# Kernel optimization log

Hardware: AMD Instinct MI355X
Metric: run time of the kernel (lower is better)

Reference implementation:

```python
import jax, jax.numpy as jnp
import numpy as np


def setup_inputs() -> dict:
    key = jax.random.key(0)
    kq, kk, kv = jax.random.split(key, 3)
    B, S, D = 8, 2048, 128
    Q = jax.random.normal(kq, (B, S, D), dtype=jnp.float32)
    K = jax.random.normal(kk, (B, S, D), dtype=jnp.float32)
    V = jax.random.normal(kv, (B, S, D), dtype=jnp.float32)
    return {"Q": Q, "K": K, "V": V}


def reference(Q, K, V):
    # scores: [B, S, S]
    d = Q.shape[-1]
    scores = jnp.einsum('bqd,bkd->bqk', Q, K) / jnp.sqrt(jnp.float32(d))
    # causal mask: position i attends to keys <= i (original sets upper triangle to -inf)
    S = scores.shape[-1]
    causal = jnp.tril(jnp.ones((S, S), dtype=bool))  # [S, S]
    scores = jnp.where(causal[None, :, :], scores, -jnp.inf)
    probs = jax.nn.softmax(scores, axis=-1)
    return jnp.einsum('bqk,bkd->bqd', probs, V)
```

## Files before the change

kernel.cpp:

```cpp
#include <hip/hip_runtime.h>

#define BB 8
#define SS 2048
#define DD 128
#define SEG ((size_t)BB * SS * DD)

typedef _Float16 f16;
typedef _Float16 f16x2 __attribute__((ext_vector_type(2)));
typedef __fp16 h16x2 __attribute__((ext_vector_type(2)));
typedef _Float16 f16x8 __attribute__((ext_vector_type(8)));
typedef float f32x4 __attribute__((ext_vector_type(4)));

#define SWV(d) ((((d) & 7) ^ (((d) >> 3) & 7)) << 3)

#define DEFER_THR 4.0f

static __device__ __forceinline__ float fast_exp2(float x) {
#if __has_builtin(__builtin_amdgcn_exp2f)
    return __builtin_amdgcn_exp2f(x);
#else
    return exp2f(x);
#endif
}

static __device__ __forceinline__ f16x2 cvt_pk(float a, float b) {
    h16x2 r = __builtin_amdgcn_cvt_pkrtz(a, b);
    return __builtin_bit_cast(f16x2, r);
}

static __device__ __forceinline__ uint2 pack4(f32x4 v) {
    f16x2 lo = cvt_pk(v[0], v[1]);
    f16x2 hi = cvt_pk(v[2], v[3]);
    uint2 u;
    u.x = __builtin_bit_cast(unsigned int, lo);
    u.y = __builtin_bit_cast(unsigned int, hi);
    return u;
}

template <int NS>
__global__ __launch_bounds__(256, 2)
void attn_fwd(const float* __restrict__ Qg, const float* __restrict__ Kg,
              const float* __restrict__ Vg, float* __restrict__ Og,
              f16* __restrict__ Opf, float2* __restrict__ mlb)
{
    __shared__ __align__(16) f16 Kl[64 * 128];
    __shared__ __align__(16) f16 Vt[128 * 64];
    __shared__ __align__(16) f16 Pl[4][16 * 64];

    const int tid  = threadIdx.x;
    const int lane = tid & 63;
    const int w    = tid >> 6;
    const int c_   = lane & 15;
    const int g    = lane >> 4;

    const int L   = blockIdx.x;
    const int bb  = L & 7;
    const int rem = L >> 3;
    const int qb  = 31 - (rem / NS);
    const int sg  = rem % NS;
    const int T   = qb + 1;
    const int t0  = (T * sg) / NS;
    const int t1  = (T * (sg + 1)) / NS;

    const int qrow0 = qb * 64 + w * 16;

    const float qs = 0.08838834764831845f * 1.4426950408889634f;
    f16x8 qf[4];
    {
        const float* qp = Qg + (size_t)(bb * SS + qrow0 + c_) * DD;
#pragma unroll
        for (int kk = 0; kk < 4; ++kk) {
            const int d0 = kk * 32 + g * 8;
            f32x4 a = *(const f32x4*)(qp + d0);
            f32x4 b = *(const f32x4*)(qp + d0 + 4);
            f16x8 q;
#pragma unroll
            for (int i = 0; i < 4; ++i) {
                q[i]     = (f16)(a[i] * qs);
                q[i + 4] = (f16)(b[i] * qs);
            }
            qf[kk] = q;
        }
    }

    f32x4 Oa[8];
#pragma unroll
    for (int i = 0; i < 8; ++i) Oa[i] = (f32x4){0.f, 0.f, 0.f, 0.f};
    float mrun[4] = {-1e30f, -1e30f, -1e30f, -1e30f};
    float lpart[4] = {0.f, 0.f, 0.f, 0.f};

    f16* Pw = &Pl[w][0];

    const int krow = tid >> 5;
    const int kc4  = tid & 31;
    const int vkg  = tid >> 5;
    const int vq   = tid & 31;

    f32x4 kreg[8], vreg[8];

    if (t0 < t1) {
        {
            const size_t gb = (size_t)(bb * SS + t0 * 64) * DD;
#pragma unroll
            for (int j = 0; j < 8; ++j)
                kreg[j] = *(const f32x4*)(Kg + gb + (krow + 8 * j) * DD + kc4 * 4);
#pragma unroll
            for (int i = 0; i < 8; ++i)
                vreg[i] = *(const f32x4*)(Vg + gb + (vkg * 8 + i) * DD + vq * 4);
        }

        for (int t = t0; t < t1; ++t) {
            __syncthreads();
#pragma unroll
            for (int j = 0; j < 8; ++j) {
                const int row = krow + 8 * j;
                const int el  = row * 128 + ((kc4 * 4) ^ ((row & 7) << 3));
                *(uint2*)&Kl[el] = pack4(kreg[j]);
            }
#pragma unroll
            for (int dd = 0; dd < 4; ++dd) {
                const int d  = vq * 4 + dd;
                const int sw = SWV(d);
#pragma unroll
                for (int h = 0; h < 2; ++h) {
                    f32x4 vv = {vreg[4 * h + 0][dd], vreg[4 * h + 1][dd],
                                vreg[4 * h + 2][dd], vreg[4 * h + 3][dd]};
                    const int el = d * 64 + ((vkg * 8 + 4 * h) ^ sw);
                    *(uint2*)&Vt[el] = pack4(vv);
                }
            }
            __syncthreads();

            if (t + 1 < t1) {
                const size_t gb = (size_t)(bb * SS + (t + 1) * 64) * DD;
#pragma unroll
                for (int j = 0; j < 8; ++j)
                    kreg[j] = *(const f32x4*)(Kg + gb + (krow + 8 * j) * DD + kc4 * 4);
#pragma unroll
                for (int i = 0; i < 8; ++i)
                    vreg[i] = *(const f32x4*)(Vg + gb + (vkg * 8 + i) * DD + vq * 4);
            }

            const int kbase = t * 64;

            f32x4 s4[4];
            __builtin_amdgcn_s_setprio(1);
#pragma unroll
            for (int nb = 0; nb < 4; ++nb) {
                f32x4 acc = (f32x4){0.f, 0.f, 0.f, 0.f};
                const int row = c_ + nb * 16;
                const int sw  = (row & 7) << 3;
#pragma unroll
                for (int kk = 0; kk < 4; ++kk) {
                    f16x8 kb = *(const f16x8*)&Kl[row * 128 + ((kk * 32 + g * 8) ^ sw)];
                    acc = __builtin_amdgcn_mfma_f32_16x16x32_f16(qf[kk], kb, acc, 0, 0, 0);
                }
                s4[nb] = acc;
            }
            __builtin_amdgcn_s_setprio(0);

            if (t == qb) {
#pragma unroll
                for (int nb = 0; nb < 4; ++nb)
#pragma unroll
                    for (int r = 0; r < 4; ++r) {
                        const int kj = kbase + nb * 16 + c_;
                        const int qi = qrow0 + g * 4 + r;
                        if (kj > qi) s4[nb][r] = -1e30f;
                    }
            }

            float wm = -1e30f;
#pragma unroll
            for (int nb = 0; nb < 4; ++nb) {
                f32x4 v = s4[nb];
                wm = fmaxf(wm, fmaxf(fmaxf(v[0], v[1]), fmaxf(v[2], v[3])));
            }
            wm = fmaxf(wm, __shfl_xor(wm, 1));
            wm = fmaxf(wm, __shfl_xor(wm, 2));
            wm = fmaxf(wm, __shfl_xor(wm, 4));
            wm = fmaxf(wm, __shfl_xor(wm, 8));
            wm = fmaxf(wm, __shfl_xor(wm, 16));
            wm = fmaxf(wm, __shfl_xor(wm, 32));
            float mrmin = fminf(fminf(mrun[0], mrun[1]), fminf(mrun[2], mrun[3]));

            if (!__all(wm - mrmin <= DEFER_THR)) {
                float sc[4];
                float scmin = 1.0f;
#pragma unroll
                for (int r = 0; r < 4; ++r) {
                    float pm = fmaxf(fmaxf(s4[0][r], s4[1][r]),
                                     fmaxf(s4[2][r], s4[3][r]));
                    pm = fmaxf(pm, __shfl_xor(pm, 1));
                    pm = fmaxf(pm, __shfl_xor(pm, 2));
                    pm = fmaxf(pm, __shfl_xor(pm, 4));
                    pm = fmaxf(pm, __shfl_xor(pm, 8));
                    const bool keep = (pm - mrun[r] <= DEFER_THR);
                    sc[r] = keep ? 1.0f : fast_exp2(mrun[r] - pm);
                    if (!keep) mrun[r] = pm;
                    scmin = fminf(scmin, sc[r]);
                }
                if (scmin < 1.0f) {
#pragma unroll
                    for (int r = 0; r < 4; ++r) {
                        lpart[r] *= sc[r];
#pragma unroll
                        for (int dblk = 0; dblk < 8; ++dblk)
                            Oa[dblk][r] *= sc[r];
                    }
                }
            }

#pragma unroll
            for (int nb = 0; nb < 4; ++nb) {
                float pv[4];
#pragma unroll
                for (int r = 0; r < 4; ++r) {
                    pv[r] = fast_exp2(s4[nb][r] - mrun[r]);
                    lpart[r] += pv[r];
                }
                f16x2 p01 = cvt_pk(pv[0], pv[1]);
                f16x2 p23 = cvt_pk(pv[2], pv[3]);
#pragma unroll
                for (int r = 0; r < 4; ++r) {
                    const int row = g * 4 + r;
                    const f16 hv = (r < 2) ? p01[r & 1] : p23[r & 1];
                    Pw[row * 64 + ((nb * 16 + c_) ^ ((row & 7) << 3))] = hv;
                }
            }

#pragma unroll
            for (int ks = 0; ks < 2; ++ks) {
                f16x8 pa = *(const f16x8*)&Pw[c_ * 64 + ((ks * 32 + g * 8) ^ ((c_ & 7) << 3))];
                __builtin_amdgcn_s_setprio(1);
#pragma unroll
                for (int dblk = 0; dblk < 8; ++dblk) {
                    const int d  = dblk * 16 + c_;
                    f16x8 vb = *(const f16x8*)&Vt[d * 64 + ((ks * 32 + g * 8) ^ SWV(d))];
                    Oa[dblk] = __builtin_amdgcn_mfma_f32_16x16x32_f16(pa, vb, Oa[dblk], 0, 0, 0);
                }
                __builtin_amdgcn_s_setprio(0);
            }
        }
    }

    float lrun[4];
#pragma unroll
    for (int r = 0; r < 4; ++r) {
        float v = lpart[r];
        v += __shfl_xor(v, 1);
        v += __shfl_xor(v, 2);
        v += __shfl_xor(v, 4);
        v += __shfl_xor(v, 8);
        lrun[r] = v;
    }

    if (NS == 1) {
#pragma unroll
        for (int r = 0; r < 4; ++r) {
            const int qrow = qrow0 + g * 4 + r;
            float* dst = Og + (size_t)(bb * SS + qrow) * DD + c_;
            const float inv = 1.0f / lrun[r];
#pragma unroll
            for (int dblk = 0; dblk < 8; ++dblk)
                dst[dblk * 16] = Oa[dblk][r] * inv;
        }
    } else {
        f16*    od  = Opf + (size_t)sg * SEG;
        float2* mld = mlb + (size_t)sg * BB * SS;
#pragma unroll
        for (int r = 0; r < 4; ++r) {
            const int qrow = qrow0 + g * 4 + r;
            f16* dst = od + (size_t)(bb * SS + qrow) * DD + c_;
#pragma unroll
            for (int dblk = 0; dblk < 8; ++dblk)
                dst[dblk * 16] = (f16)Oa[dblk][r];
            if (c_ == 0) mld[bb * SS + qrow] = make_float2(mrun[r], lrun[r]);
        }
    }
}

template <int NS>
__global__ __launch_bounds__(256)
void merge_kernel(float* __restrict__ out, const f16* __restrict__ Opf,
                  const float2* __restrict__ mlb)
{
    const int idx = blockIdx.x * 256 + threadIdx.x;
    const int row = idx >> 4;
    float2 ml[NS];
#pragma unroll
    for (int i = 0; i < NS; ++i) ml[i] = mlb[(size_t)i * BB * SS + row];
    float mm = ml[0].x;
#pragma unroll
    for (int i = 1; i < NS; ++i) mm = fmaxf(mm, ml[i].x);
    float e[NS], den = 0.f;
#pragma unroll
    for (int i = 0; i < NS; ++i) {
        e[i] = fast_exp2(ml[i].x - mm);
        den += ml[i].y * e[i];
    }
    const float inv = 1.0f / den;

    float acc[8] = {0.f, 0.f, 0.f, 0.f, 0.f, 0.f, 0.f, 0.f};
#pragma unroll
    for (int i = 0; i < NS; ++i) {
        f16x8 v = *(const f16x8*)(Opf + (size_t)i * SEG + (size_t)idx * 8);
#pragma unroll
        for (int j = 0; j < 8; ++j) acc[j] += (float)v[j] * e[i];
    }
    float4 o0, o1;
    o0.x = acc[0] * inv; o0.y = acc[1] * inv; o0.z = acc[2] * inv; o0.w = acc[3] * inv;
    o1.x = acc[4] * inv; o1.y = acc[5] * inv; o1.z = acc[6] * inv; o1.w = acc[7] * inv;
    float4* dst = (float4*)(out + (size_t)idx * 8);
    dst[0] = o0;
    dst[1] = o1;
}

extern "C" void kernel_launch(void* const* d_in, const int* in_sizes, int n_in,
                              void* d_out, int out_size, void* d_ws, size_t ws_size,
                              hipStream_t stream)
{
    const float* Q = (const float*)d_in[0];
    const float* K = (const float*)d_in[1];
    const float* V = (const float*)d_in[2];
    float* out = (float*)d_out;

    const size_t OPB = SEG * sizeof(f16);
    const size_t MLB = (size_t)BB * SS * sizeof(float2);
    const int mergeGrid = (int)(SEG / 8 / 256);

    const size_t need8 = 8 * OPB + 8 * MLB;
    const size_t need4 = 4 * OPB + 4 * MLB;

    if (ws_size >= need8) {
        f16*    Opf = (f16*)d_ws;
        float2* mlb = (float2*)((char*)d_ws + 8 * OPB);
        hipLaunchKernelGGL((attn_fwd<8>), dim3(8 * 32 * 8), dim3(256), 0, stream,
                           Q, K, V, out, Opf, mlb);
        hipLaunchKernelGGL((merge_kernel<8>), dim3(mergeGrid), dim3(256), 0, stream,
                           out, Opf, mlb);
    } else if (ws_size >= need4) {
        f16*    Opf = (f16*)d_ws;
        float2* mlb = (float2*)((char*)d_ws + 4 * OPB);
        hipLaunchKernelGGL((attn_fwd<4>), dim3(8 * 32 * 4), dim3(256), 0, stream,
                           Q, K, V, out, Opf, mlb);
        hipLaunchKernelGGL((merge_kernel<4>), dim3(mergeGrid), dim3(256), 0, stream,
                           out, Opf, mlb);
    } else {
        hipLaunchKernelGGL((attn_fwd<1>), dim3(8 * 32), dim3(256), 0, stream,
                           Q, K, V, out, (f16*)nullptr, (float2*)nullptr);
    }
}
```

Before: 113.8 us.

## Double-buffer K/V tiles in LDS and drop the eight-way split-KV path

K and V shared-memory tiles are now double-buffered. The next tile is converted and staged into the alternate buffer between the QK and PV phases, and global loads run two tiles ahead. This cuts the loop from two barriers per iteration to one and overlaps staging with MFMA work. The NS=8 split path is removed, so launches default to four splits, which means fewer blocks and less merge traffic but possibly lower occupancy. LDS use roughly doubles to about 80KB per block, which may limit the two-blocks-per-CU launch bound.

Measured after the change: 103.6 us. -8.9%, faster.

```diff
diff --git a/kernel.cpp b/kernel.cpp
--- a/kernel.cpp
+++ b/kernel.cpp
@@ -43,8 +43,8 @@
               const float* __restrict__ Vg, float* __restrict__ Og,
               f16* __restrict__ Opf, float2* __restrict__ mlb)
 {
-    __shared__ __align__(16) f16 Kl[64 * 128];
-    __shared__ __align__(16) f16 Vt[128 * 64];
+    __shared__ __align__(16) f16 Kl[2][64 * 128];
+    __shared__ __align__(16) f16 Vt[2][128 * 64];
     __shared__ __align__(16) f16 Pl[4][16 * 64];
 
     const int tid  = threadIdx.x;
@@ -98,49 +98,53 @@
 
     f32x4 kreg[8], vreg[8];
 
+#define LOADT(tt)                                                              \
+    {                                                                          \
+        const size_t gb = (size_t)(bb * SS + (tt) * 64) * DD;                  \
+        _Pragma("unroll")                                                      \
+        for (int j = 0; j < 8; ++j)                                            \
+            kreg[j] = *(const f32x4*)(Kg + gb + (krow + 8 * j) * DD + kc4 * 4);\
+        _Pragma("unroll")                                                      \
+        for (int i = 0; i < 8; ++i)                                            \
+            vreg[i] = *(const f32x4*)(Vg + gb + (vkg * 8 + i) * DD + vq * 4);  \
+    }
+
+#define STAGE_K(pb_)                                                           \
+    {                                                                          \
+        _Pragma("unroll")                                                      \
+        for (int j = 0; j < 8; ++j) {                                          \
+            const int row = krow + 8 * j;                                      \
+            const int el  = row * 128 + ((kc4 * 4) ^ ((row & 7) << 3));        \
+            *(uint2*)&Kl[pb_][el] = pack4(kreg[j]);                            \
+        }                                                                      \
+    }
+
+#define STAGE_V(pb_)                                                           \
+    {                                                                          \
+        _Pragma("unroll")                                                      \
+        for (int dd = 0; dd < 4; ++dd) {                                       \
+            const int d  = vq * 4 + dd;                                        \
+            const int sw = SWV(d);                                             \
+            _Pragma("unroll")                                                  \
+            for (int h = 0; h < 2; ++h) {                                      \
+                f32x4 vv = {vreg[4 * h + 0][dd], vreg[4 * h + 1][dd],          \
+                            vreg[4 * h + 2][dd], vreg[4 * h + 3][dd]};         \
+                const int el = d * 64 + ((vkg * 8 + 4 * h) ^ sw);              \
+                *(uint2*)&Vt[pb_][el] = pack4(vv);                             \
+            }                                                                  \
+        }                                                                      \
+    }
+
     if (t0 < t1) {
-        {
-            const size_t gb = (size_t)(bb * SS + t0 * 64) * DD;
-#pragma unroll
-            for (int j = 0; j < 8; ++j)
-                kreg[j] = *(const f32x4*)(Kg + gb + (krow + 8 * j) * DD + kc4 * 4);
-#pragma unroll
-            for (int i = 0; i < 8; ++i)
-                vreg[i] = *(const f32x4*)(Vg + gb + (vkg * 8 + i) * DD + vq * 4);
-        }
+        LOADT(t0);
+        STAGE_K(t0 & 1);
+        STAGE_V(t0 & 1);
+        if (t0 + 1 < t1) LOADT(t0 + 1);
+        __syncthreads();
 
         for (int t = t0; t < t1; ++t) {
-            __syncthreads();
-#pragma unroll
-            for (int j = 0; j < 8; ++j) {
-                const int row = krow + 8 * j;
-                const int el  = row * 128 + ((kc4 * 4) ^ ((row & 7) << 3));
-                *(uint2*)&Kl[el] = pack4(kreg[j]);
-            }
-#pragma unroll
-            for (int dd = 0; dd < 4; ++dd) {
-                const int d  = vq * 4 + dd;
-                const int sw = SWV(d);
-#pragma unroll
-                for (int h = 0; h < 2; ++h) {
-                    f32x4 vv = {vreg[4 * h + 0][dd], vreg[4 * h + 1][dd],
-                                vreg[4 * h + 2][dd], vreg[4 * h + 3][dd]};
-                    const int el = d * 64 + ((vkg * 8 + 4 * h) ^ sw);
-                    *(uint2*)&Vt[el] = pack4(vv);
-                }
-            }
-            __syncthreads();
-
-            if (t + 1 < t1) {
-                const size_t gb = (size_t)(bb * SS + (t + 1) * 64) * DD;
-#pragma unroll
-                for (int j = 0; j < 8; ++j)
-                    kreg[j] = *(const f32x4*)(Kg + gb + (krow + 8 * j) * DD + kc4 * 4);
-#pragma unroll
-                for (int i = 0; i < 8; ++i)
-                    vreg[i] = *(const f32x4*)(Vg + gb + (vkg * 8 + i) * DD + vq * 4);
-            }
-
+            const int pb = t & 1;
+            const bool more = (t + 1 < t1);
             const int kbase = t * 64;
 
             f32x4 s4[4];
@@ -152,12 +156,14 @@
                 const int sw  = (row & 7) << 3;
 #pragma unroll
                 for (int kk = 0; kk < 4; ++kk) {
-                    f16x8 kb = *(const f16x8*)&Kl[row * 128 + ((kk * 32 + g * 8) ^ sw)];
+                    f16x8 kb = *(const f16x8*)&Kl[pb][row * 128 + ((kk * 32 + g * 8) ^ sw)];
                     acc = __builtin_amdgcn_mfma_f32_16x16x32_f16(qf[kk], kb, acc, 0, 0, 0);
                 }
                 s4[nb] = acc;
             }
             __builtin_amdgcn_s_setprio(0);
+
+            if (more) STAGE_K(pb ^ 1);
 
             if (t == qb) {
 #pragma unroll
@@ -229,6 +235,8 @@
                 }
             }
 
+            if (more) STAGE_V(pb ^ 1);
+
 #pragma unroll
             for (int ks = 0; ks < 2; ++ks) {
                 f16x8 pa = *(const f16x8*)&Pw[c_ * 64 + ((ks * 32 + g * 8) ^ ((c_ & 7) << 3))];
@@ -236,11 +244,14 @@
 #pragma unroll
                 for (int dblk = 0; dblk < 8; ++dblk) {
                     const int d  = dblk * 16 + c_;
-                    f16x8 vb = *(const f16x8*)&Vt[d * 64 + ((ks * 32 + g * 8) ^ SWV(d))];
+                    f16x8 vb = *(const f16x8*)&Vt[pb][d * 64 + ((ks * 32 + g * 8) ^ SWV(d))];
                     Oa[dblk] = __builtin_amdgcn_mfma_f32_16x16x32_f16(pa, vb, Oa[dblk], 0, 0, 0);
                 }
                 __builtin_amdgcn_s_setprio(0);
             }
+
+            if (t + 2 < t1) LOADT(t + 2);
+            if (more) __syncthreads();
         }
     }
 
@@ -329,17 +340,9 @@
     const size_t MLB = (size_t)BB * SS * sizeof(float2);
     const int mergeGrid = (int)(SEG / 8 / 256);
 
-    const size_t need8 = 8 * OPB + 8 * MLB;
     const size_t need4 = 4 * OPB + 4 * MLB;
 
-    if (ws_size >= need8) {
-        f16*    Opf = (f16*)d_ws;
-        float2* mlb = (float2*)((char*)d_ws + 8 * OPB);
-        hipLaunchKernelGGL((attn_fwd<8>), dim3(8 * 32 * 8), dim3(256), 0, stream,
-                           Q, K, V, out, Opf, mlb);
-        hipLaunchKernelGGL((merge_kernel<8>), dim3(mergeGrid), dim3(256), 0, stream,
-                           out, Opf, mlb);
-    } else if (ws_size >= need4) {
+    if (ws_size >= need4) {
         f16*    Opf = (f16*)d_ws;
         float2* mlb = (float2*)((char*)d_ws + 4 * OPB);
         hipLaunchKernelGGL((attn_fwd<4>), dim3(8 * 32 * 4), dim3(256), 0, stream,
```
